# Kernel optimization log

Measured on AMD Instinct MI355X. Metric: run time of the kernel, lower is better.

## Reference

```python
import jax, jax.numpy as jnp
import numpy as np

N_HEAD = 12


def setup_inputs() -> dict:
    key = jax.random.key(0)
    k1, k2, k3 = jax.random.split(key, 3)
    B, T, C = 4, 1024, 768
    x = jax.random.normal(k1, (B, T, C), dtype=jnp.float32)
    # torch Linear weight is (out,in); we store transposed so y = x @ W
    w_attn = jax.random.normal(k2, (C, 3 * C), dtype=jnp.float32) * (1.0 / np.sqrt(C))
    w_proj = jax.random.normal(k3, (C, C), dtype=jnp.float32) * (1.0 / np.sqrt(C))
    return {"x": x, "w_attn": w_attn, "w_proj": w_proj}


def reference(x, w_attn, w_proj):
    B, T, C = x.shape
    nh = N_HEAD
    hs = C // nh
    b = 0.01

    qkv = (x @ w_attn).reshape(B, T, 3, nh, hs)
    # per-head-dim standardization; torch.std default is unbiased (ddof=1)
    mu = qkv.mean(axis=-1, keepdims=True)
    sd = jnp.std(qkv, axis=-1, ddof=1, keepdims=True)
    qkv = (qkv - mu) / sd

    # time-leading for scan: (T, B, nh, hs)
    q = jnp.transpose(qkv[:, :, 0], (1, 0, 2, 3))
    k = jnp.transpose(qkv[:, :, 1], (1, 0, 2, 3))
    v = jnp.transpose(qkv[:, :, 2], (1, 0, 2, 3))

    eye = jnp.eye(hs, dtype=x.dtype) * 0.99  # hs_eye

    def step(S, qkv_t):
        q_t, k_t, v_t = qkv_t  # each (B, nh, hs)
        # L_t = 0.99*I - b * k k^T ; I_t = k v^T  (computed on the fly, not materialized over T)
        L_t = eye - b * jnp.einsum('bhi,bhj->bhij', k_t, k_t)
        I_t = jnp.einsum('bhi,bhj->bhij', k_t, v_t)
        S = jnp.einsum('bhij,bhjk->bhik', S, L_t) + I_t
        o_t = jnp.einsum('bhj,bhij->bhi', q_t, S)
        return S, o_t

    S0 = jnp.zeros((B, nh, hs, hs), dtype=x.dtype)
    _, vt = jax.lax.scan(step, S0, (q, k, v))  # vt: (T, B, nh, hs)

    y = jnp.transpose(vt, (1, 0, 2, 3)).reshape(B, T, C) @ w_proj
    return x + y
```

## Files before the change

### kernel.cpp

```cpp
#include <hip/hip_runtime.h>

typedef unsigned short u16;
typedef __attribute__((ext_vector_type(4))) unsigned short u16x4;
typedef __attribute__((ext_vector_type(8))) short bf16x8;
typedef __attribute__((ext_vector_type(4))) float f32x4;

#define B_ 4
#define T_ 1024
#define NH 12
#define HS 64
#define CDIM 768
#define QKVW 2304
#define NC 16
#define CS 64
#define LAM 0.99f
#define BP  (0.01f/0.99f)
#define MROWS 4096
#define LSTR 72

#define OFF_WPT 4718592
#define OFF_W  9437184
#define OFF_U  (OFF_W  + 768*4096)
#define OFF_C  (OFF_U  + 768*4096)
#define OFF_R0 (OFF_C  + 768*4096)
#define OFF_XB (OFF_W)
#define OFF_WAT (OFF_W + 1572864)

__device__ __forceinline__ u16 f2bf(float f) {
    union { float f; unsigned u; } a; a.f = f;
    const unsigned r = a.u + 0x7FFF + ((a.u >> 16) & 1);
    return (u16)(r >> 16);
}
__device__ __forceinline__ float bf2f(u16 h) {
    union { unsigned u; float f; } a; a.u = ((unsigned)h) << 16; return a.f;
}
__device__ __forceinline__ u16x4 f2bf4(const f32x4 v) {
    u16x4 u; u.x = f2bf(v[0]); u.y = f2bf(v[1]); u.z = f2bf(v[2]); u.w = f2bf(v[3]);
    return u;
}
__device__ __forceinline__ int swz(int row, int col) {
    return row * 64 + (((col >> 3) ^ (row & 7)) << 3) + (col & 7);
}

__device__ __forceinline__ void tcast_body(const float* __restrict__ src,
                                           u16* __restrict__ dst,
                                           int Cn, int Rr, int bx, int by) {
    const int ln = threadIdx.x & 63, kg = threadIdx.x >> 6;
    const int n = bx * 64 + ln;
    const int kb = by * 64 + kg * 16;
    u16 tmp[16];
#pragma unroll
    for (int j = 0; j < 16; ++j)
        tmp[j] = f2bf(src[(size_t)(kb + j) * Cn + n]);
#pragma unroll
    for (int j4 = 0; j4 < 4; ++j4) {
        u16x4 u; u.x = tmp[j4*4]; u.y = tmp[j4*4+1]; u.z = tmp[j4*4+2]; u.w = tmp[j4*4+3];
        *(u16x4*)&dst[(size_t)n * Rr + kb + j4*4] = u;
    }
}

__global__ __launch_bounds__(256)
void cast_all_kernel(const float* __restrict__ x, const float* __restrict__ wa,
                     const float* __restrict__ wp, u16* __restrict__ xb,
                     u16* __restrict__ waT, u16* __restrict__ wpT) {
    const int bid = blockIdx.x;
    if (bid < 3072) {
        const size_t i = ((size_t)bid * 256 + threadIdx.x) * 4;
        const float4 v = *(const float4*)(x + i);
        u16x4 u;
        u.x = f2bf(v.x); u.y = f2bf(v.y); u.z = f2bf(v.z); u.w = f2bf(v.w);
        *(u16x4*)(xb + i) = u;
    } else if (bid < 3504) {
        const int idx = bid - 3072;
        tcast_body(wa, waT, QKVW, CDIM, idx % 36, idx / 36);
    } else {
        const int idx = bid - 3504;
        tcast_body(wp, wpT, CDIM, CDIM, idx % 12, idx / 12);
    }
}

__device__ __forceinline__ void gll16(const u16* g, u16* lds) {
    __builtin_amdgcn_global_load_lds(
        (const __attribute__((address_space(1))) unsigned*)g,
        (__attribute__((address_space(3))) unsigned*)lds, 16, 0, 0);
}

template<bool ADD_RES, bool NORM, int MI_T, int MINW, int XC, int RW, int RH>
__global__ __launch_bounds__(256, MINW)
void gemm_mfma(const u16* __restrict__ A, const u16* __restrict__ Bt,
               const float* __restrict__ R, void* __restrict__ Cout,
               int N, int K) {
    __shared__ u16 As[32 * MI_T * 64];
    __shared__ u16 Bs[128 * 64];
    const int tid  = threadIdx.x;
    const int wave = tid >> 6, lane = tid & 63;
    const int wm = wave >> 1, wn = wave & 1;
    const int ln = lane & 15, quad = lane >> 4;

    const int bid = blockIdx.x;
    const int xcd = bid & 7, slot = bid >> 3;
    const int tx = (xcd % XC) * RW + slot % RW;
    const int ty = (xcd / XC) * RH + slot / RW;
    const int m0 = ty * (32 * MI_T), n0 = tx * 128;

    const int rl = lane >> 3;
    const int kx = ((lane & 7) ^ rl) * 8;
    const u16* Ag = A + (size_t)(m0 + wave * (8 * MI_T) + rl) * K + kx;
    const u16* Bg = Bt + (size_t)(n0 + wave * 32 + rl) * K + kx;
    u16* AsW = &As[(wave * (8 * MI_T)) * 64];
    u16* BsW = &Bs[(wave * 32) * 64];

    f32x4 acc[MI_T][4] = {};

    for (int k0 = 0; k0 < K; k0 += 64) {
        __syncthreads();
#pragma unroll
        for (int c8 = 0; c8 < MI_T; ++c8)
            gll16(Ag + (size_t)(c8 * 8) * K + k0, AsW + c8 * 8 * 64);
#pragma unroll
        for (int c8 = 0; c8 < 4; ++c8)
            gll16(Bg + (size_t)(c8 * 8) * K + k0, BsW + c8 * 8 * 64);
        __syncthreads();
#pragma unroll
        for (int k32 = 0; k32 < 64; k32 += 32) {
            const int ko = (k32 + quad * 8) ^ ((ln & 7) * 8);
            bf16x8 af[MI_T], bfr[4];
#pragma unroll
            for (int mi = 0; mi < MI_T; ++mi)
                af[mi] = *(const bf16x8*)&As[(wm * (16 * MI_T) + mi * 16 + ln) * 64 + ko];
#pragma unroll
            for (int ni = 0; ni < 4; ++ni)
                bfr[ni] = *(const bf16x8*)&Bs[(wn * 64 + ni * 16 + ln) * 64 + ko];
#pragma unroll
            for (int mi = 0; mi < MI_T; ++mi)
#pragma unroll
                for (int ni = 0; ni < 4; ++ni)
                    acc[mi][ni] = __builtin_amdgcn_mfma_f32_16x16x32_bf16(
                        af[mi], bfr[ni], acc[mi][ni], 0, 0, 0);
        }
    }

#pragma unroll
    for (int mi = 0; mi < MI_T; ++mi) {
        const int rb = m0 + wm * (16 * MI_T) + mi * 16 + quad * 4;
#pragma unroll
        for (int r = 0; r < 4; ++r) {
            if (NORM) {
                const float a0 = acc[mi][0][r], a1 = acc[mi][1][r];
                const float a2 = acc[mi][2][r], a3 = acc[mi][3][r];
                float s1 = a0 + a1 + a2 + a3;
                float s2 = a0*a0 + a1*a1 + a2*a2 + a3*a3;
#pragma unroll
                for (int m = 1; m < 16; m <<= 1) {
                    s1 += __shfl_xor(s1, m, 64);
                    s2 += __shfl_xor(s2, m, 64);
                }
                const float mu = s1 * (1.0f / 64.0f);
                const float rs = rsqrtf((s2 - 64.0f * mu * mu) * (1.0f / 63.0f));
                u16* op = (u16*)Cout + (size_t)(rb + r) * N + n0 + wn * 64 + ln;
                op[0]  = f2bf((a0 - mu) * rs);
                op[16] = f2bf((a1 - mu) * rs);
                op[32] = f2bf((a2 - mu) * rs);
                op[48] = f2bf((a3 - mu) * rs);
            } else {
#pragma unroll
                for (int ni = 0; ni < 4; ++ni) {
                    const int col = n0 + wn * 64 + ni * 16 + ln;
                    float v = acc[mi][ni][r];
                    if (ADD_RES) v += R[(size_t)(rb + r) * N + col];
                    ((float*)Cout)[(size_t)(rb + r) * N + col] = v;
                }
            }
        }
    }
}

template<bool ASWZ, bool BSWZ, int NT>
__device__ __forceinline__ void mm_stripN(const u16* A, const u16* Bq,
                                          int wr, int ln, int quad, f32x4 (&acc)[NT]) {
#pragma unroll
    for (int k0 = 0; k0 < 64; k0 += 32) {
        const int kq = k0 + quad * 8;
        const int ks = kq ^ ((ln & 7) * 8);
        const bf16x8 a = ASWZ ? *(const bf16x8*)&A[(wr + ln) * 64 + ks]
                              : *(const bf16x8*)&A[(wr + ln) * LSTR + kq];
#pragma unroll
        for (int nt = 0; nt < NT; ++nt) {
            const bf16x8 b = BSWZ ? *(const bf16x8*)&Bq[(nt * 16 + ln) * 64 + ks]
                                  : *(const bf16x8*)&Bq[(nt * 16 + ln) * LSTR + kq];
            acc[nt] = __builtin_amdgcn_mfma_f32_16x16x32_bf16(a, b, acc[nt], 0, 0, 0);
        }
    }
}

template<bool ASWZ, bool BSWZ>
__device__ __forceinline__ void mm_strip2(const u16* A, const u16* Bq,
                                          int wr, int ln, int quad, f32x4 (&acc)[4]) {
    mm_stripN<ASWZ, BSWZ, 4>(A, Bq, wr, ln, quad, acc);
}

__global__ __launch_bounds__(256, 4)
void chunkA(const u16* __restrict__ qkv, float* __restrict__ ws,
            u16* __restrict__ wbg, u16* __restrict__ ktg) {
    __shared__ u16 Kb[4096], Vb[4096], KT[4096], VT[4096], NT[4096];
    u16* const Yb = Kb;
    u16* const Np = Vb;
    u16* const UT = NT;
    u16* const HbT = VT;

    const int cc = blockIdx.x;
    const int bh = cc >> 4, c = cc & 15;
    const int b = bh / NH, h = bh - b * NH;
    const int tid = threadIdx.x;
    const int w = tid >> 6, lane = tid & 63;
    const int ln = lane & 15, quad = lane >> 4;
    const int wr = w * 16;
    const u16* base = qkv + ((size_t)(b * T_ + c * CS)) * QKVW + h * HS;

    {
        const int tr0 = w * 4 + quad;
        const int d0 = ln * 4;
        float vsc = __powf(LAM, -(float)(tr0 + 1));
        const float v16 = __powf(LAM, -16.0f);
#pragma unroll
        for (int p = 0; p < 4; ++p) {
            const int t = p * 16 + tr0;
            const u16x4 k4 = *(const u16x4*)(base + (size_t)t * QKVW + CDIM + d0);
            const u16x4 vu = *(const u16x4*)(base + (size_t)t * QKVW + 2 * CDIM + d0);
            u16x4 v4; v4.x = f2bf(bf2f(vu.x) * vsc); v4.y = f2bf(bf2f(vu.y) * vsc);
            v4.z = f2bf(bf2f(vu.z) * vsc); v4.w = f2bf(bf2f(vu.w) * vsc);
            *(u16x4*)&Kb[swz(t, d0)] = k4;
            *(u16x4*)&Vb[swz(t, d0)] = v4;
            KT[swz(d0 + 0, t)] = k4.x; KT[swz(d0 + 1, t)] = k4.y;
            KT[swz(d0 + 2, t)] = k4.z; KT[swz(d0 + 3, t)] = k4.w;
            VT[swz(d0 + 0, t)] = v4.x; VT[swz(d0 + 1, t)] = v4.y;
            VT[swz(d0 + 2, t)] = v4.z; VT[swz(d0 + 3, t)] = v4.w;
            vsc *= v16;
        }
    }
    __syncthreads();

    f32x4 accG[4] = {}, accH[4] = {}, c1[4] = {};
    mm_strip2<true,true>(Kb, Kb, wr, ln, quad, accG);
    mm_strip2<true,true>(Kb, Vb, wr, ln, quad, accH);
    mm_strip2<true,true>(VT, KT, wr, ln, quad, c1);
    __syncthreads();

#pragma unroll
    for (int nt = 0; nt < 4; ++nt) {
        const int col = nt * 16 + ln;
        u16x4 nvT, hvT;
#pragma unroll
        for (int r = 0; r < 4; ++r) {
            const int row = wr + quad * 4 + r;
            const float g = accG[nt][r];
            const u16 nv = (col < row) ? f2bf(BP * g) : (u16)0;
            Np[swz(row, col)] = nv;
            Yb[swz(row, col)] = (row == col) ? f2bf(1.0f)
                               : ((col < row) ? f2bf(-BP * g) : (u16)0);
            ((u16*)&nvT)[r] = nv;
            ((u16*)&hvT)[r] = (col < row) ? f2bf(accH[nt][r]) : (u16)0;
        }
        *(u16x4*)&NT[swz(col, wr + quad * 4)] = nvT;
        *(u16x4*)&HbT[swz(col, wr + quad * 4)] = hvT;
    }
    __syncthreads();

    for (int j = 0; j < 3; ++j) {
        f32x4 sq[4] = {};
        mm_strip2<true,true>(Np, NT, wr, ln, quad, sq);
        __syncthreads();
#pragma unroll
        for (int nt = 0; nt < 4; ++nt) {
            const int col = nt * 16 + ln;
            u16x4 sv;
#pragma unroll
            for (int r = 0; r < 4; ++r) {
                const u16 v = f2bf(sq[nt][r]);
                Np[swz(wr + quad * 4 + r, col)] = v;
                ((u16*)&sv)[r] = v;
            }
            *(u16x4*)&NT[swz(col, wr + quad * 4)] = sv;
        }
        __syncthreads();
        f32x4 ya[4];
#pragma unroll
        for (int nt = 0; nt < 4; ++nt)
#pragma unroll
            for (int r = 0; r < 4; ++r)
                ya[nt][r] = bf2f(Yb[swz(wr + quad * 4 + r, nt * 16 + ln)]);
        mm_strip2<true,true>(Yb, NT, wr, ln, quad, ya);
#pragma unroll
        for (int nt = 0; nt < 4; ++nt)
#pragma unroll
            for (int r = 0; r < 4; ++r)
                Yb[swz(wr + quad * 4 + r, nt * 16 + ln)] = f2bf(ya[nt][r]);
    }

    u16* Ugp = (u16*)(ws + OFF_U) + (size_t)cc * 4096;
    u16* Cgp = (u16*)(ws + OFF_C) + (size_t)cc * 4096;

    f32x4 wv[4] = {};
    mm_strip2<true,true>(Yb, KT, wr, ln, quad, wv);

    f32x4 m1[4] = {};
    mm_strip2<true,true>(Yb, HbT, wr, ln, quad, m1);
#pragma unroll
    for (int nt = 0; nt < 4; ++nt)
#pragma unroll
        for (int r = 0; r < 4; ++r)
            Np[swz(wr + quad * 4 + r, nt * 16 + ln)] = f2bf(m1[nt][r]);

#pragma unroll
    for (int nt = 0; nt < 4; ++nt)
#pragma unroll
        for (int r = 0; r < 4; ++r)
            Yb[swz(wr + quad * 4 + r, nt * 16 + ln)] = f2bf(wv[nt][r]);

    f32x4 uv[4] = {};
    mm_strip2<true,true>(Np, KT, wr, ln, quad, uv);
#pragma unroll
    for (int nt = 0; nt < 4; ++nt)
        *(u16x4*)&Ugp[(size_t)(w * 64 + lane) * 16 + nt * 4] = f2bf4(uv[nt]);
    __syncthreads();
#pragma unroll
    for (int nt = 0; nt < 4; ++nt)
        *(u16x4*)&UT[swz(nt * 16 + ln, wr + quad * 4)] = f2bf4(uv[nt]);
    __syncthreads();

    f32x4 c2[4] = {};
    mm_strip2<true,true>(KT, UT, wr, ln, quad, c2);
#pragma unroll
    for (int nt = 0; nt < 4; ++nt) {
        const f32x4 cv = c1[nt] - BP * c2[nt];
        *(u16x4*)&Cgp[(size_t)(w * 64 + lane) * 16 + nt * 4] = f2bf4(cv);
    }

    for (int e = tid; e < 512; e += 256) {
        *(bf16x8*)&wbg[(size_t)cc * 4096 + e * 8] = *(const bf16x8*)&Yb[e * 8];
        *(bf16x8*)&ktg[(size_t)cc * 4096 + e * 8] = *(const bf16x8*)&KT[e * 8];
    }
}

__global__ __launch_bounds__(256)
void chunkB(float* __restrict__ ws, const u16* __restrict__ wbg,
            const u16* __restrict__ ktg) {
    __shared__ u16 WBs[2][4096], KTs[2][4096];
    __shared__ u16 RTb[16 * LSTR], PTb[16 * LSTR];

    const int bid = blockIdx.x;
    const int bh = bid >> 2, qtr = bid & 3;
    const int cb = qtr * 16;
    const int tid = threadIdx.x;
    const int w = tid >> 6, lane = tid & 63;
    const int ln = lane & 15, quad = lane >> 4;
    const int wr = w * 16;
    const float lam64 = __powf(LAM, 64.0f);
    u16* r0tg = (u16*)(ws + OFF_R0);

    f32x4 R[1] = {};

    for (int e = tid; e < 16 * LSTR; e += 256) RTb[e] = 0;

    const int off = w * 1024;
    {
        const size_t b0 = (size_t)(bh * 16) * 4096;
#pragma unroll
        for (int i = 0; i < 2; ++i) {
            gll16(wbg + b0 + off + i * 512 + lane * 8, &WBs[0][off + i * 512]);
            gll16(ktg + b0 + off + i * 512 + lane * 8, &KTs[0][off + i * 512]);
        }
    }
    __syncthreads();

    for (int c = 0; c < NC; ++c) {
        const int buf = c & 1;
        const size_t cc = (size_t)(bh * 16 + c);

        if (c + 1 < NC) {
            const size_t b1 = (cc + 1) * 4096;
#pragma unroll
            for (int i = 0; i < 2; ++i) {
                gll16(wbg + b1 + off + i * 512 + lane * 8, &WBs[buf ^ 1][off + i * 512]);
                gll16(ktg + b1 + off + i * 512 + lane * 8, &KTs[buf ^ 1][off + i * 512]);
            }
        }

        const u16* Cg = (const u16*)(ws + OFF_C) + cc * 4096
                        + (size_t)(w * 64 + lane) * 16 + qtr * 4;
        const u16x4 cu = *(const u16x4*)Cg;

        f32x4 p[1] = {};
        mm_stripN<true,false,1>(&WBs[buf][0], RTb, wr, ln, quad, p);
        *(u16x4*)&PTb[ln * LSTR + wr + quad * 4] = f2bf4(p[0]);
        __syncthreads();

        f32x4 kp[1] = {};
        mm_stripN<true,false,1>(&KTs[buf][0], PTb, wr, ln, quad, kp);

        u16* r0t = r0tg + cc * 4096;
        const int swzr = (wr + quad * 4) ^ ((ln & 7) * 8);
        const int x = cb + ln;
        *(u16x4*)&r0t[x * 64 + swzr] = f2bf4(R[0]);
        f32x4 cv; cv[0] = bf2f(cu.x); cv[1] = bf2f(cu.y);
        cv[2] = bf2f(cu.z); cv[3] = bf2f(cu.w);
        R[0] = lam64 * (R[0] - BP * kp[0] + cv);
        *(u16x4*)&RTb[ln * LSTR + wr + quad * 4] = f2bf4(R[0]);
        __syncthreads();
    }
}

__global__ __launch_bounds__(256, 3)
void chunkC(const u16* __restrict__ qkv, float* __restrict__ ws,
            const u16* __restrict__ wbg, const u16* __restrict__ ktg,
            u16* __restrict__ ob) {
    __shared__ u16 Wb[4096], KTb[4096];
    __shared__ u16 RuT[64 * LSTR];
    __shared__ u16 Qhb[64 * LSTR], Kb[64 * LSTR], Vtb[64 * LSTR];
    u16* const R0Tb = RuT;
    u16* const RmTb = RuT;
    u16* const A1m = Kb;
    u16* const A2m = Vtb;

    const int cc = blockIdx.x;
    const int bh = cc >> 4, c = cc & 15;
    const int b = bh / NH, h = bh - b * NH;
    const int tid = threadIdx.x;
    const int w = tid >> 6, lane = tid & 63;
    const int ln = lane & 15, quad = lane >> 4;
    const int wr = w * 16;
    const u16* base = qkv + ((size_t)(b * T_ + c * CS)) * QKVW + h * HS;
    const u16* r0tg = (const u16*)(ws + OFF_R0);

    const int off = w * 1024;
    {
        const size_t bb = (size_t)cc * 4096;
#pragma unroll
        for (int i = 0; i < 2; ++i) {
            gll16(wbg  + bb + off + i * 512 + lane * 8, &Wb[off + i * 512]);
            gll16(ktg  + bb + off + i * 512 + lane * 8, &KTb[off + i * 512]);
            gll16(r0tg + bb + off + i * 512 + lane * 8, &R0Tb[off + i * 512]);
        }
    }
    {
        const int tr0 = w * 4 + quad;
        const int d0 = ln * 4;
        float qsc = __powf(LAM, (float)(tr0 + 1));
        float vsc = 1.0f / qsc;
        const float q16 = __powf(LAM, 16.0f);
        const float v16 = 1.0f / q16;
#pragma unroll
        for (int p = 0; p < 4; ++p) {
            const int t = p * 16 + tr0;
            const u16x4 qu = *(const u16x4*)(base + (size_t)t * QKVW + d0);
            const u16x4 ku = *(const u16x4*)(base + (size_t)t * QKVW + CDIM + d0);
            const u16x4 vu = *(const u16x4*)(base + (size_t)t * QKVW + 2 * CDIM + d0);
            u16x4 q4; q4.x = f2bf(bf2f(qu.x) * qsc); q4.y = f2bf(bf2f(qu.y) * qsc);
            q4.z = f2bf(bf2f(qu.z) * qsc); q4.w = f2bf(bf2f(qu.w) * qsc);
            u16x4 v4; v4.x = f2bf(bf2f(vu.x) * vsc); v4.y = f2bf(bf2f(vu.y) * vsc);
            v4.z = f2bf(bf2f(vu.z) * vsc); v4.w = f2bf(bf2f(vu.w) * vsc);
            *(u16x4*)&Qhb[t * LSTR + d0] = q4;
            *(u16x4*)&Kb[t * LSTR + d0] = ku;
            *(u16x4*)&Vtb[t * LSTR + d0] = v4;
            qsc *= q16; vsc *= v16;
        }
    }
    __syncthreads();

    const u16* Ugp = (const u16*)(ws + OFF_U) + (size_t)cc * 4096
                     + (size_t)(w * 64 + lane) * 16;
    const bf16x8 uu0 = *(const bf16x8*)&Ugp[0];
    const bf16x8 uu1 = *(const bf16x8*)&Ugp[8];

    f32x4 a1[4] = {}, a2[4] = {};
    mm_strip2<false,false>(Qhb, Kb,   wr, ln, quad, a1);
    mm_strip2<false,false>(Qhb, Vtb,  wr, ln, quad, a2);
    __syncthreads();

    const int row = wr + quad * 4;
#pragma unroll
    for (int nt = 0; nt < 4; ++nt) {
        const int col = nt * 16 + ln;
#pragma unroll
        for (int r = 0; r < 4; ++r) {
            const int t = row + r;
            A1m[t * LSTR + col] = (col <= t) ? f2bf(a1[nt][r]) : (u16)0;
            A2m[t * LSTR + col] = (col <= t) ? f2bf(a2[nt][r]) : (u16)0;
        }
    }

    f32x4 Oacc[4] = {}, wr0[4] = {};
    mm_strip2<false,true >(Qhb, R0Tb, wr, ln, quad, Oacc);
    mm_strip2<true ,true >(Wb,  R0Tb, wr, ln, quad, wr0);
#pragma unroll
    for (int nt = 0; nt < 4; ++nt) {
        const bf16x8 uu = (nt < 2) ? uu0 : uu1;
        const int o = (nt & 1) * 4;
        wr0[nt][0] += bf2f((u16)uu[o + 0]); wr0[nt][1] += bf2f((u16)uu[o + 1]);
        wr0[nt][2] += bf2f((u16)uu[o + 2]); wr0[nt][3] += bf2f((u16)uu[o + 3]);
    }
    __syncthreads();

#pragma unroll
    for (int nt = 0; nt < 4; ++nt)
        *(u16x4*)&RmTb[(nt * 16 + ln) * LSTR + row] = f2bf4(wr0[nt]);
    __syncthreads();

    f32x4 O3[4] = {};
    mm_strip2<false,true >(A2m, KTb,  wr, ln, quad, Oacc);
    mm_strip2<false,false>(A1m, RmTb, wr, ln, quad, O3);

#pragma unroll
    for (int nt = 0; nt < 4; ++nt) {
        const int col = nt * 16 + ln;
#pragma unroll
        for (int r = 0; r < 4; ++r) {
            const float o = Oacc[nt][r] - BP * O3[nt][r];
            ob[((size_t)(b * T_ + c * CS + row + r)) * CDIM + h * HS + col] = f2bf(o);
        }
    }
}

extern "C" void kernel_launch(void* const* d_in, const int* in_sizes, int n_in,
                              void* d_out, int out_size, void* d_ws, size_t ws_size,
                              hipStream_t stream) {
    const float* x      = (const float*)d_in[0];
    const float* w_attn = (const float*)d_in[1];
    const float* w_proj = (const float*)d_in[2];
    float* ws  = (float*)d_ws;
    u16* qkv = (u16*)ws;
    u16* xb  = (u16*)(ws + OFF_XB);
    u16* waT = (u16*)(ws + OFF_WAT);
    u16* wpT = (u16*)(ws + OFF_WPT);
    u16* ob  = (u16*)(ws + OFF_C);
    u16* wbg = (u16*)d_out;
    u16* ktg = (u16*)d_out + 768 * 4096;

    cast_all_kernel<<<3648, 256, 0, stream>>>(x, w_attn, w_proj, xb, waT, wpT);

    gemm_mfma<false, true, 2, 4, 2, 9, 16><<<1152, 256, 0, stream>>>(
        xb, waT, nullptr, qkv, QKVW, CDIM);

    chunkA<<<768, 256, 0, stream>>>(qkv, ws, wbg, ktg);
    chunkB<<<192, 256, 0, stream>>>(ws, wbg, ktg);
    chunkC<<<768, 256, 0, stream>>>(qkv, ws, wbg, ktg, ob);

    gemm_mfma<true, false, 2, 4, 1, 6, 8><<<384, 256, 0, stream>>>(
        ob, wpT, x, (float*)d_out, CDIM, CDIM);
}
```

Baseline: 157.0 us.

## Fuse x bf16 cast into QKV GEMM A-load and compact chunkC LDS

The first GEMM now reads fp32 x directly and converts to bf16 while staging into LDS, removing the separate x cast pass and its bf16 round-trip through memory. The cast kernel shrinks to the weight transposes only. chunkC switches from padded LDS rows to XOR-swizzled 64-wide tiles, aliases buffers so shared memory is smaller, and raises its occupancy target from 3 to 4. It also defers the KT load until the buffer it reuses is free. The fp32 A path uses plain register loads instead of direct-to-LDS loads, which adds conversion work and register pressure inside the GEMM loop.

```diff
diff --git a/kernel.cpp b/kernel.cpp
--- a/kernel.cpp
+++ b/kernel.cpp
@@ -23,7 +23,6 @@
 #define OFF_U  (OFF_W  + 768*4096)
 #define OFF_C  (OFF_U  + 768*4096)
 #define OFF_R0 (OFF_C  + 768*4096)
-#define OFF_XB (OFF_W)
 #define OFF_WAT (OFF_W + 1572864)
 
 __device__ __forceinline__ u16 f2bf(float f) {
@@ -60,21 +59,13 @@
 }
 
 __global__ __launch_bounds__(256)
-void cast_all_kernel(const float* __restrict__ x, const float* __restrict__ wa,
-                     const float* __restrict__ wp, u16* __restrict__ xb,
-                     u16* __restrict__ waT, u16* __restrict__ wpT) {
+void cast_w_kernel(const float* __restrict__ wa, const float* __restrict__ wp,
+                   u16* __restrict__ waT, u16* __restrict__ wpT) {
     const int bid = blockIdx.x;
-    if (bid < 3072) {
-        const size_t i = ((size_t)bid * 256 + threadIdx.x) * 4;
-        const float4 v = *(const float4*)(x + i);
-        u16x4 u;
-        u.x = f2bf(v.x); u.y = f2bf(v.y); u.z = f2bf(v.z); u.w = f2bf(v.w);
-        *(u16x4*)(xb + i) = u;
-    } else if (bid < 3504) {
-        const int idx = bid - 3072;
-        tcast_body(wa, waT, QKVW, CDIM, idx % 36, idx / 36);
+    if (bid < 432) {
+        tcast_body(wa, waT, QKVW, CDIM, bid % 36, bid / 36);
     } else {
-        const int idx = bid - 3504;
+        const int idx = bid - 432;
         tcast_body(wp, wpT, CDIM, CDIM, idx % 12, idx / 12);
     }
 }
@@ -85,9 +76,10 @@
         (__attribute__((address_space(3))) unsigned*)lds, 16, 0, 0);
 }
 
-template<bool ADD_RES, bool NORM, int MI_T, int MINW, int XC, int RW, int RH>
+template<bool ADD_RES, bool NORM, bool AF32, int MI_T, int MINW, int XC, int RW, int RH>
 __global__ __launch_bounds__(256, MINW)
-void gemm_mfma(const u16* __restrict__ A, const u16* __restrict__ Bt,
+void gemm_mfma(const u16* __restrict__ A, const float* __restrict__ Af,
+               const u16* __restrict__ Bt,
                const float* __restrict__ R, void* __restrict__ Cout,
                int N, int K) {
     __shared__ u16 As[32 * MI_T * 64];
@@ -105,7 +97,10 @@
 
     const int rl = lane >> 3;
     const int kx = ((lane & 7) ^ rl) * 8;
-    const u16* Ag = A + (size_t)(m0 + wave * (8 * MI_T) + rl) * K + kx;
+    const u16*   Ag  = AF32 ? nullptr
+                            : A  + (size_t)(m0 + wave * (8 * MI_T) + rl) * K + kx;
+    const float* Axg = AF32 ? Af + (size_t)(m0 + wave * (8 * MI_T) + rl) * K + kx
+                            : nullptr;
     const u16* Bg = Bt + (size_t)(n0 + wave * 32 + rl) * K + kx;
     u16* AsW = &As[(wave * (8 * MI_T)) * 64];
     u16* BsW = &Bs[(wave * 32) * 64];
@@ -115,11 +110,27 @@
     for (int k0 = 0; k0 < K; k0 += 64) {
         __syncthreads();
 #pragma unroll
-        for (int c8 = 0; c8 < MI_T; ++c8)
-            gll16(Ag + (size_t)(c8 * 8) * K + k0, AsW + c8 * 8 * 64);
-#pragma unroll
         for (int c8 = 0; c8 < 4; ++c8)
             gll16(Bg + (size_t)(c8 * 8) * K + k0, BsW + c8 * 8 * 64);
+        if (AF32) {
+#pragma unroll
+            for (int c8 = 0; c8 < MI_T; ++c8) {
+                const float* src = Axg + (size_t)(c8 * 8) * K + k0;
+                const float4 f0 = *(const float4*)(src);
+                const float4 f1 = *(const float4*)(src + 4);
+                u16x4 lo, hi;
+                lo.x = f2bf(f0.x); lo.y = f2bf(f0.y);
+                lo.z = f2bf(f0.z); lo.w = f2bf(f0.w);
+                hi.x = f2bf(f1.x); hi.y = f2bf(f1.y);
+                hi.z = f2bf(f1.z); hi.w = f2bf(f1.w);
+                u16* dst = AsW + c8 * 8 * 64 + lane * 8;
+                *(u16x4*)dst = lo; *(u16x4*)(dst + 4) = hi;
+            }
+        } else {
+#pragma unroll
+            for (int c8 = 0; c8 < MI_T; ++c8)
+                gll16(Ag + (size_t)(c8 * 8) * K + k0, AsW + c8 * 8 * 64);
+        }
         __syncthreads();
 #pragma unroll
         for (int k32 = 0; k32 < 64; k32 += 32) {
@@ -410,15 +421,13 @@
     }
 }
 
-__global__ __launch_bounds__(256, 3)
+__global__ __launch_bounds__(256, 4)
 void chunkC(const u16* __restrict__ qkv, float* __restrict__ ws,
             const u16* __restrict__ wbg, const u16* __restrict__ ktg,
             u16* __restrict__ ob) {
-    __shared__ u16 Wb[4096], KTb[4096];
-    __shared__ u16 RuT[64 * LSTR];
-    __shared__ u16 Qhb[64 * LSTR], Kb[64 * LSTR], Vtb[64 * LSTR];
-    u16* const R0Tb = RuT;
-    u16* const RmTb = RuT;
+    __shared__ u16 Wb[4096], R0Tb[4096], Qhb[4096], Kb[4096], Vtb[4096];
+    u16* const RmTb = Wb;
+    u16* const KTb  = Qhb;
     u16* const A1m = Kb;
     u16* const A2m = Vtb;
 
@@ -433,12 +442,11 @@
     const u16* r0tg = (const u16*)(ws + OFF_R0);
 
     const int off = w * 1024;
+    const size_t bb = (size_t)cc * 4096;
     {
-        const size_t bb = (size_t)cc * 4096;
 #pragma unroll
         for (int i = 0; i < 2; ++i) {
             gll16(wbg  + bb + off + i * 512 + lane * 8, &Wb[off + i * 512]);
-            gll16(ktg  + bb + off + i * 512 + lane * 8, &KTb[off + i * 512]);
             gll16(r0tg + bb + off + i * 512 + lane * 8, &R0Tb[off + i * 512]);
         }
     }
@@ -459,22 +467,22 @@
             q4.z = f2bf(bf2f(qu.z) * qsc); q4.w = f2bf(bf2f(qu.w) * qsc);
             u16x4 v4; v4.x = f2bf(bf2f(vu.x) * vsc); v4.y = f2bf(bf2f(vu.y) * vsc);
             v4.z = f2bf(bf2f(vu.z) * vsc); v4.w = f2bf(bf2f(vu.w) * vsc);
-            *(u16x4*)&Qhb[t * LSTR + d0] = q4;
-            *(u16x4*)&Kb[t * LSTR + d0] = ku;
-            *(u16x4*)&Vtb[t * LSTR + d0] = v4;
+            *(u16x4*)&Qhb[swz(t, d0)] = q4;
+            *(u16x4*)&Kb[swz(t, d0)] = ku;
+            *(u16x4*)&Vtb[swz(t, d0)] = v4;
             qsc *= q16; vsc *= v16;
         }
     }
     __syncthreads();
 
-    const u16* Ugp = (const u16*)(ws + OFF_U) + (size_t)cc * 4096
+    const u16* Ugp = (const u16*)(ws + OFF_U) + bb
                      + (size_t)(w * 64 + lane) * 16;
     const bf16x8 uu0 = *(const bf16x8*)&Ugp[0];
     const bf16x8 uu1 = *(const bf16x8*)&Ugp[8];
 
     f32x4 a1[4] = {}, a2[4] = {};
-    mm_strip2<false,false>(Qhb, Kb,   wr, ln, quad, a1);
-    mm_strip2<false,false>(Qhb, Vtb,  wr, ln, quad, a2);
+    mm_strip2<true,true>(Qhb, Kb,  wr, ln, quad, a1);
+    mm_strip2<true,true>(Qhb, Vtb, wr, ln, quad, a2);
     __syncthreads();
 
     const int row = wr + quad * 4;
@@ -484,14 +492,14 @@
 #pragma unroll
         for (int r = 0; r < 4; ++r) {
             const int t = row + r;
-            A1m[t * LSTR + col] = (col <= t) ? f2bf(a1[nt][r]) : (u16)0;
-            A2m[t * LSTR + col] = (col <= t) ? f2bf(a2[nt][r]) : (u16)0;
+            A1m[swz(t, col)] = (col <= t) ? f2bf(a1[nt][r]) : (u16)0;
+            A2m[swz(t, col)] = (col <= t) ? f2bf(a2[nt][r]) : (u16)0;
         }
     }
 
     f32x4 Oacc[4] = {}, wr0[4] = {};
-    mm_strip2<false,true >(Qhb, R0Tb, wr, ln, quad, Oacc);
-    mm_strip2<true ,true >(Wb,  R0Tb, wr, ln, quad, wr0);
+    mm_strip2<true,true>(Qhb, R0Tb, wr, ln, quad, Oacc);
+    mm_strip2<true,true>(Wb,  R0Tb, wr, ln, quad, wr0);
 #pragma unroll
     for (int nt = 0; nt < 4; ++nt) {
         const bf16x8 uu = (nt < 2) ? uu0 : uu1;
@@ -502,13 +510,16 @@
     __syncthreads();
 
 #pragma unroll
+    for (int i = 0; i < 2; ++i)
+        gll16(ktg + bb + off + i * 512 + lane * 8, &KTb[off + i * 512]);
+#pragma unroll
     for (int nt = 0; nt < 4; ++nt)
-        *(u16x4*)&RmTb[(nt * 16 + ln) * LSTR + row] = f2bf4(wr0[nt]);
+        *(u16x4*)&RmTb[swz(nt * 16 + ln, row)] = f2bf4(wr0[nt]);
     __syncthreads();
 
     f32x4 O3[4] = {};
-    mm_strip2<false,true >(A2m, KTb,  wr, ln, quad, Oacc);
-    mm_strip2<false,false>(A1m, RmTb, wr, ln, quad, O3);
+    mm_strip2<true,true>(A2m, KTb,  wr, ln, quad, Oacc);
+    mm_strip2<true,true>(A1m, RmTb, wr, ln, quad, O3);
 
 #pragma unroll
     for (int nt = 0; nt < 4; ++nt) {
@@ -529,22 +540,21 @@
     const float* w_proj = (const float*)d_in[2];
     float* ws  = (float*)d_ws;
     u16* qkv = (u16*)ws;
-    u16* xb  = (u16*)(ws + OFF_XB);
     u16* waT = (u16*)(ws + OFF_WAT);
     u16* wpT = (u16*)(ws + OFF_WPT);
     u16* ob  = (u16*)(ws + OFF_C);
     u16* wbg = (u16*)d_out;
     u16* ktg = (u16*)d_out + 768 * 4096;
 
-    cast_all_kernel<<<3648, 256, 0, stream>>>(x, w_attn, w_proj, xb, waT, wpT);
-
-    gemm_mfma<false, true, 2, 4, 2, 9, 16><<<1152, 256, 0, stream>>>(
-        xb, waT, nullptr, qkv, QKVW, CDIM);
+    cast_w_kernel<<<576, 256, 0, stream>>>(w_attn, w_proj, waT, wpT);
+
+    gemm_mfma<false, true, true, 2, 4, 2, 9, 16><<<1152, 256, 0, stream>>>(
+        nullptr, x, waT, nullptr, qkv, QKVW, CDIM);
 
     chunkA<<<768, 256, 0, stream>>>(qkv, ws, wbg, ktg);
     chunkB<<<192, 256, 0, stream>>>(ws, wbg, ktg);
     chunkC<<<768, 256, 0, stream>>>(qkv, ws, wbg, ktg, ob);
 
-    gemm_mfma<true, false, 2, 4, 1, 6, 8><<<384, 256, 0, stream>>>(
-        ob, wpT, x, (float*)d_out, CDIM, CDIM);
-}
+    gemm_mfma<true, false, false, 2, 4, 1, 6, 8><<<384, 256, 0, stream>>>(
+        ob, nullptr, wpT, x, (float*)d_out, CDIM, CDIM);
+}
```

After: 158.3 us. Within noise of the previous version (+0.8%).
